# Kernel optimization log

Measured on AMD Instinct MI355X. Metric: run time of the kernel, lower is better.

The kernel has to match this reference:

```python
import jax, jax.numpy as jnp
import numpy as np

N_EMBD = 2048
QKV_EMBD = 2048
N_HEAD = 32
N_KV_HEAD = 8
HEAD_DIM = QKV_EMBD // N_HEAD  # 64
GROUPS = N_HEAD // N_KV_HEAD   # 4
ROPE_THETA = 10000.0
SCALE = float(np.sqrt(HEAD_DIM))


def setup_inputs() -> dict:
    key = jax.random.key(0)
    ks = jax.random.split(key, 12)
    B, S = 2, 2048
    inp = {
        "query": jax.random.normal(ks[0], (B, S, N_EMBD), jnp.float32),
        "key": jax.random.normal(ks[1], (B, S, N_EMBD), jnp.float32),
        "value": jax.random.normal(ks[2], (B, S, N_EMBD), jnp.float32),
        "mask": jnp.ones((B, S), dtype=bool),
        "Wq": jax.random.normal(ks[3], (QKV_EMBD, N_EMBD), jnp.float32) * 0.02,
        "bq": jnp.zeros((QKV_EMBD,), jnp.float32),
        "Wk": jax.random.normal(ks[4], (N_KV_HEAD * HEAD_DIM, N_EMBD), jnp.float32) * 0.02,
        "bk": jnp.zeros((N_KV_HEAD * HEAD_DIM,), jnp.float32),
        "Wv": jax.random.normal(ks[5], (N_KV_HEAD * HEAD_DIM, N_EMBD), jnp.float32) * 0.02,
        "bv": jnp.zeros((N_KV_HEAD * HEAD_DIM,), jnp.float32),
        "Wo": jax.random.normal(ks[6], (N_EMBD, QKV_EMBD), jnp.float32) * 0.02,
        "bo": jnp.zeros((N_EMBD,), jnp.float32),
    }
    return inp


def _rotate_half(x):
    d = x.shape[-1] // 2
    return jnp.concatenate([-x[..., d:], x[..., :d]], axis=-1)


def _rope_cos_sin(seq_len, dtype):
    # rope_factor == 1.0 -> no NTK adjustment; is_causal -> position_ids = arange
    inv_freq = 1.0 / (ROPE_THETA ** (jnp.arange(0, HEAD_DIM, 2, dtype=jnp.float32) / HEAD_DIM))
    pos = jnp.arange(seq_len, dtype=jnp.float32)
    freqs = jnp.einsum("i,j->ij", pos, inv_freq)           # [S, D/2]
    emb = jnp.concatenate([freqs, freqs], axis=-1)          # [S, D]
    return jnp.cos(emb).astype(dtype)[None, None], jnp.sin(emb).astype(dtype)[None, None]


def reference(query, key, value, mask, Wq, bq, Wk, bk, Wv, bv, Wo, bo):
    B, S, _ = query.shape
    Q = (query @ Wq.T + bq).reshape(B, S, N_HEAD, HEAD_DIM).transpose(0, 2, 1, 3)      # [B,H,S,D]
    K = (key @ Wk.T + bk).reshape(B, S, N_KV_HEAD, HEAD_DIM).transpose(0, 2, 1, 3)     # [B,KV,S,D]
    V = (value @ Wv.T + bv).reshape(B, S, N_KV_HEAD, HEAD_DIM).transpose(0, 2, 1, 3)

    cos, sin = _rope_cos_sin(S, Q.dtype)
    Q = Q * cos + _rotate_half(Q) * sin
    K = K * cos + _rotate_half(K) * sin

    # interleaved GQA repeat: each kv head serves GROUPS consecutive query heads
    K = jnp.repeat(K, GROUPS, axis=1)  # [B,H,S,D]
    V = jnp.repeat(V, GROUPS, axis=1)

    attn = jnp.einsum("bhqd,bhkd->bhqk", Q, K)              # [B,H,S,S]
    causal = jnp.tril(jnp.ones((S, S), dtype=bool))
    full_mask = mask[:, None, None, :] & causal[None, None]  # [B,1,S,S]
    attn = jnp.where(full_mask, attn, jnp.finfo(attn.dtype).min)
    attn_weights = jax.nn.softmax(attn / SCALE, axis=-1)     # dropout p=0 (eval)
    out = jnp.einsum("bhqk,bhkd->bhqd", attn_weights, V)
    out = out.transpose(0, 2, 1, 3).reshape(B, S, QKV_EMBD)
    return out @ Wo.T + bo
```

## Files before the change

### kernel.cpp

```cpp
#include <hip/hip_runtime.h>
#include <hip/hip_bf16.h>
#include <cmath>

#define NE   2048
#define NH   32
#define NKV  8
#define HD   64
#define SEQ  2048
#define NB   2

typedef __attribute__((ext_vector_type(4))) float f32x4;
typedef __attribute__((ext_vector_type(16))) float f32x16;
typedef __attribute__((ext_vector_type(8))) short bf16x8;
typedef __attribute__((ext_vector_type(4))) short bf16x4;

typedef const __attribute__((address_space(1))) void cgvoid;
typedef __attribute__((address_space(3))) void lvoid;

#define QSCALE 0.18033688011112042f

__device__ __forceinline__ short f2bf(float f) {
  union { float f; unsigned u; } v; v.f = f;
  unsigned r = v.u + 0x7fffu + ((v.u >> 16) & 1u);
  return (short)(r >> 16);
}

__device__ __forceinline__ unsigned cvt_pk_bf16(float a, float b) {
  unsigned r;
  asm("v_cvt_pk_bf16_f32 %0, %1, %2" : "=v"(r) : "v"(a), "v"(b));
  return r;
}

__global__ __launch_bounds__(256) void cvt_all(
    const float* __restrict__ s0, short* __restrict__ d0,
    const float* __restrict__ s1, short* __restrict__ d1,
    const float* __restrict__ s2, short* __restrict__ d2,
    const float* __restrict__ s3, short* __restrict__ d3,
    const float* __restrict__ s4, short* __restrict__ d4,
    const float* __restrict__ s5, short* __restrict__ d5,
    const float* __restrict__ s6, short* __restrict__ d6)
{
  int idx = blockIdx.x * 256 + threadIdx.x;
  const float* s; short* d; int rel;
  if      (idx < 1048576) { s = s0; d = d0; rel = idx; }
  else if (idx < 2097152) { s = s1; d = d1; rel = idx - 1048576; }
  else if (idx < 3145728) { s = s2; d = d2; rel = idx - 2097152; }
  else if (idx < 3670016) { s = s3; d = d3; rel = idx - 3145728; }
  else if (idx < 3801088) { s = s4; d = d4; rel = idx - 3670016; }
  else if (idx < 3932160) { s = s5; d = d5; rel = idx - 3801088; }
  else                    { s = s6; d = d6; rel = idx - 3932160; }
  size_t off = (size_t)rel * 8;
  f32x4 a = *(const f32x4*)(s + off);
  f32x4 b = *(const f32x4*)(s + off + 4);
  bf16x8 o;
  #pragma unroll
  for (int j = 0; j < 4; ++j) { o[j] = f2bf(a[j]); o[4 + j] = f2bf(b[j]); }
  *(bf16x8*)(d + off) = o;
}

template<int EPI>
__device__ __forceinline__ void gemm_body(
    short* As, short* Ws, int m0, int n0,
    const short* __restrict__ A, const short* __restrict__ W,
    const float* __restrict__ bias, void* __restrict__ Cout,
    int N, int K)
{
  const int t = threadIdx.x, lane = t & 63, w = t >> 6;
  const int lr = lane & 15, lg = lane >> 4;
  const int wm = (w >> 1) * 64, wn = (w & 1) * 64;

  f32x4 acc[4][4];
  #pragma unroll
  for (int i = 0; i < 4; ++i)
    #pragma unroll
    for (int j = 0; j < 4; ++j) acc[i][j] = (f32x4){0.f, 0.f, 0.f, 0.f};

  const int nt = K >> 6;

  #pragma unroll
  for (int it = 0; it < 4; ++it) {
    int e = it * 256 + t, r = e >> 3, c = e & 7;
    int cs = ((c ^ (r & 7)) << 3);
    __builtin_amdgcn_global_load_lds((cgvoid*)(A + (size_t)(m0 + r) * K + cs),
                                     (lvoid*)(As + e * 8), 16, 0, 0);
    __builtin_amdgcn_global_load_lds((cgvoid*)(W + (size_t)(n0 + r) * K + cs),
                                     (lvoid*)(Ws + e * 8), 16, 0, 0);
  }

  for (int ti = 0; ti < nt; ++ti) {
    const int cur = ti & 1;
    const short* Ab = As + cur * 8192;
    const short* Wb = Ws + cur * 8192;
    if (ti + 1 < nt) {
      const int k0 = (ti + 1) << 6;
      short* An = As + (cur ^ 1) * 8192;
      short* Wn = Ws + (cur ^ 1) * 8192;
      #pragma unroll
      for (int it = 0; it < 4; ++it) {
        int e = it * 256 + t, r = e >> 3, c = e & 7;
        int cs = ((c ^ (r & 7)) << 3);
        __builtin_amdgcn_global_load_lds((cgvoid*)(A + (size_t)(m0 + r) * K + k0 + cs),
                                         (lvoid*)(An + e * 8), 16, 0, 0);
        __builtin_amdgcn_global_load_lds((cgvoid*)(W + (size_t)(n0 + r) * K + k0 + cs),
                                         (lvoid*)(Wn + e * 8), 16, 0, 0);
      }
      asm volatile("s_waitcnt vmcnt(8)" ::: "memory");
    } else {
      asm volatile("s_waitcnt vmcnt(0)" ::: "memory");
    }
    __builtin_amdgcn_s_barrier();

    bf16x8 af[2][4], wf[2][4];
    #pragma unroll
    for (int ks = 0; ks < 2; ++ks)
      #pragma unroll
      for (int mf = 0; mf < 4; ++mf) {
        int row = wm + mf * 16 + lr;
        af[ks][mf] = *(const bf16x8*)(Ab + row * 64 + (((ks * 4 + lg) ^ (row & 7)) << 3));
      }
    #pragma unroll
    for (int ks = 0; ks < 2; ++ks)
      #pragma unroll
      for (int nf = 0; nf < 4; ++nf) {
        int row = wn + nf * 16 + lr;
        wf[ks][nf] = *(const bf16x8*)(Wb + row * 64 + (((ks * 4 + lg) ^ (row & 7)) << 3));
      }
    __builtin_amdgcn_s_setprio(1);
    #pragma unroll
    for (int ks = 0; ks < 2; ++ks)
      #pragma unroll
      for (int mf = 0; mf < 4; ++mf)
        #pragma unroll
        for (int nf = 0; nf < 4; ++nf)
          acc[mf][nf] = __builtin_amdgcn_mfma_f32_16x16x32_bf16(af[ks][mf], wf[ks][nf], acc[mf][nf], 0, 0, 0);
    __builtin_amdgcn_s_setprio(0);
    __builtin_amdgcn_s_barrier();
  }

  if (EPI == 0) {
    float* C = (float*)Cout;
    #pragma unroll
    for (int mf = 0; mf < 4; ++mf)
      #pragma unroll
      for (int nf = 0; nf < 4; ++nf)
        #pragma unroll
        for (int i = 0; i < 4; ++i) {
          int m = m0 + wm + mf * 16 + lg * 4 + i;
          int n = n0 + wn + nf * 16 + lr;
          C[(size_t)m * N + n] = acc[mf][nf][i] + bias[n];
        }
  } else if (EPI == 1) {
    short* C = (short*)Cout;
    #pragma unroll
    for (int mf = 0; mf < 4; ++mf)
      #pragma unroll
      for (int nf = 0; nf < 4; ++nf) {
        int n = n0 + wn + nf * 16 + lr;
        int kv = n >> 6, d = n & 63;
        int mb = m0 + wm + mf * 16 + lg * 4;
        int b = mb >> 11, s = mb & (SEQ - 1);
        bf16x4 pb;
        #pragma unroll
        for (int i = 0; i < 4; ++i) pb[i] = f2bf(acc[mf][nf][i] + bias[n]);
        *(bf16x4*)(C + (((size_t)b * NKV + kv) * HD + d) * SEQ + s) = pb;
      }
  } else {
    const int HN = (EPI == 2) ? NH : NKV;
    short* C = (short*)Cout;
    #pragma unroll
    for (int mf = 0; mf < 4; ++mf)
      #pragma unroll
      for (int nf2 = 0; nf2 < 2; ++nf2)
        #pragma unroll
        for (int i = 0; i < 4; ++i) {
          int m = m0 + wm + mf * 16 + lg * 4 + i;
          int b = m >> 11, s = m & (SEQ - 1);
          int n1 = n0 + wn + nf2 * 16 + lr;
          int n2 = n1 + 32;
          float v1 = acc[mf][nf2][i] + bias[n1];
          float v2 = acc[mf][nf2 + 2][i] + bias[n2];
          int d1 = n1 & 63;
          float inv = exp2f(-(float)d1 * (13.287712379549449f / 32.0f));
          float ang = (float)s * inv;
          float c, sn;
          __sincosf(ang, &sn, &c);
          float o1 = v1 * c - v2 * sn;
          float o2 = v2 * c + v1 * sn;
          if (EPI == 2) { o1 *= QSCALE; o2 *= QSCALE; }
          int h = n1 >> 6;
          size_t base = (((size_t)b * HN + h) * SEQ + s) * HD;
          C[base + d1]      = f2bf(o1);
          C[base + d1 + 32] = f2bf(o2);
        }
  }
}

template<int EPI>
__global__ __launch_bounds__(256) void gemm_bf16(
    const short* __restrict__ A, const short* __restrict__ W,
    const float* __restrict__ bias, void* __restrict__ Cout, int N, int K)
{
  __shared__ __align__(16) short As[2 * 128 * 64];
  __shared__ __align__(16) short Ws[2 * 128 * 64];
  gemm_body<EPI>(As, Ws, blockIdx.x * 128, blockIdx.y * 128, A, W, bias, Cout, N, K);
}

__global__ __launch_bounds__(256) void gemm_qkv(
    const short* __restrict__ qA, const short* __restrict__ Wq,
    const float* __restrict__ bq, short* __restrict__ Qout,
    const short* __restrict__ kA, const short* __restrict__ Wk,
    const float* __restrict__ bk, short* __restrict__ Kout,
    const short* __restrict__ vA, const short* __restrict__ Wv,
    const float* __restrict__ bv, short* __restrict__ Vout)
{
  __shared__ __align__(16) short As[2 * 128 * 64];
  __shared__ __align__(16) short Ws[2 * 128 * 64];
  int bid = blockIdx.x;
  if (bid < 512) {
    gemm_body<2>(As, Ws, (bid & 31) * 128, (bid >> 5) * 128, qA, Wq, bq, (void*)Qout, NE, NE);
  } else if (bid < 640) {
    int b2 = bid - 512;
    gemm_body<3>(As, Ws, (b2 & 31) * 128, (b2 >> 5) * 128, kA, Wk, bk, (void*)Kout, NKV * HD, NE);
  } else {
    int b2 = bid - 640;
    gemm_body<1>(As, Ws, (b2 & 31) * 128, (b2 >> 5) * 128, vA, Wv, bv, (void*)Vout, NKV * HD, NE);
  }
}

__global__ __launch_bounds__(256) void attn_kernel(
    const short* __restrict__ Q, const short* __restrict__ K,
    const short* __restrict__ Vt, short* __restrict__ O)
{
  __shared__ __align__(16) short Ks[2][64 * 64];
  __shared__ __align__(16) short Vs[2][64 * 64];

  const int t = threadIdx.x, lane = t & 63, w = t >> 6;
  const int l31 = lane & 31, hi = lane >> 5;
  const int by = blockIdx.y;
  const int b = by >> 3, kvh = by & 7;
  const int h = kvh * 4 + w;

  const short* Qh = Q + ((size_t)b * NH + h) * SEQ * HD;
  const short* Kh = K + ((size_t)b * NKV + kvh) * SEQ * HD;
  const short* Vh = Vt + ((size_t)b * NKV + kvh) * (size_t)HD * SEQ;

  #pragma unroll 1
  for (int pass = 0; pass < 2; ++pass) {
    const int qb32 = pass ? blockIdx.x : (63 - blockIdx.x);
    const int q0 = qb32 * 32;
    const int ntile = (qb32 >> 1) + 1;
    const int qpos = q0 + l31;

    bf16x8 qfr[4];
    #pragma unroll
    for (int dd = 0; dd < 4; ++dd)
      qfr[dd] = *(const bf16x8*)(Qh + (size_t)(q0 + l31) * HD + dd * 16 + hi * 8);

    f32x16 o[2];
    #pragma unroll
    for (int dh = 0; dh < 2; ++dh)
      #pragma unroll
      for (int r = 0; r < 16; ++r) o[dh][r] = 0.f;
    float lsum = 0.f;

    #pragma unroll
    for (int it = 0; it < 2; ++it) {
      int cid = it * 256 + t;
      int r = cid >> 3, c = cid & 7;
      int cs = ((c ^ (r & 7)) << 3);
      __builtin_amdgcn_global_load_lds((cgvoid*)(Kh + (size_t)r * HD + cs),
                                       (lvoid*)(Ks[0] + cid * 8), 16, 0, 0);
      __builtin_amdgcn_global_load_lds((cgvoid*)(Vh + (size_t)r * SEQ + cs),
                                       (lvoid*)(Vs[0] + cid * 8), 16, 0, 0);
    }
    __syncthreads();

    for (int ti = 0; ti < ntile; ++ti) {
      const int cur = ti & 1;
      if (ti + 1 < ntile) {
        const int kvn = (ti + 1) * 64;
        #pragma unroll
        for (int it = 0; it < 2; ++it) {
          int cid = it * 256 + t;
          int r = cid >> 3, c = cid & 7;
          int cs = ((c ^ (r & 7)) << 3);
          __builtin_amdgcn_global_load_lds((cgvoid*)(Kh + (size_t)(kvn + r) * HD + cs),
                                           (lvoid*)(Ks[cur ^ 1] + cid * 8), 16, 0, 0);
          __builtin_amdgcn_global_load_lds((cgvoid*)(Vh + (size_t)r * SEQ + kvn + cs),
                                           (lvoid*)(Vs[cur ^ 1] + cid * 8), 16, 0, 0);
        }
      }
      const int kv0 = ti * 64;
      const short* Kb = Ks[cur];
      const short* Vb = Vs[cur];

      f32x16 p[2];
      __builtin_amdgcn_s_setprio(1);
      #pragma unroll
      for (int f = 0; f < 2; ++f) {
        f32x16 z;
        #pragma unroll
        for (int r = 0; r < 16; ++r) z[r] = 0.f;
        #pragma unroll
        for (int dd = 0; dd < 4; ++dd) {
          int row = f * 32 + l31;
          bf16x8 ka = *(const bf16x8*)(Kb + row * 64 + (((2 * dd + hi) ^ (row & 7)) << 3));
          z = __builtin_amdgcn_mfma_f32_32x32x16_bf16(ka, qfr[dd], z, 0, 0, 0);
        }
        p[f] = z;
      }
      __builtin_amdgcn_s_setprio(0);

      if (ti == ntile - 1) {
        #pragma unroll
        for (int f = 0; f < 2; ++f)
          #pragma unroll
          for (int r = 0; r < 16; ++r) {
            int kpos = kv0 + f * 32 + (r & 3) + 8 * (r >> 2) + 4 * hi;
            if (kpos > qpos) p[f][r] = -INFINITY;
          }
      }

      unsigned pa[4][4];
      #pragma unroll
      for (int f = 0; f < 2; ++f) {
        float e[16];
        #pragma unroll
        for (int r = 0; r < 16; ++r) {
          e[r] = __builtin_amdgcn_exp2f(p[f][r]);
          lsum += e[r];
        }
        unsigned c[8];
        #pragma unroll
        for (int i = 0; i < 8; ++i) c[i] = cvt_pk_bf16(e[2 * i], e[2 * i + 1]);
        asm volatile("v_permlane32_swap_b32 %0, %1" : "+v"(c[0]), "+v"(c[2]));
        asm volatile("v_permlane32_swap_b32 %0, %1" : "+v"(c[1]), "+v"(c[3]));
        asm volatile("v_permlane32_swap_b32 %0, %1" : "+v"(c[4]), "+v"(c[6]));
        asm volatile("v_permlane32_swap_b32 %0, %1" : "+v"(c[5]), "+v"(c[7]));
        pa[2 * f][0] = c[0]; pa[2 * f][1] = c[1]; pa[2 * f][2] = c[2]; pa[2 * f][3] = c[3];
        pa[2 * f + 1][0] = c[4]; pa[2 * f + 1][1] = c[5];
        pa[2 * f + 1][2] = c[6]; pa[2 * f + 1][3] = c[7];
      }

      __builtin_amdgcn_s_setprio(1);
      #pragma unroll
      for (int ks = 0; ks < 4; ++ks) {
        bf16x8 paf = *(const bf16x8*)&pa[ks][0];
        #pragma unroll
        for (int dh = 0; dh < 2; ++dh) {
          int row = dh * 32 + l31;
          bf16x8 vb = *(const bf16x8*)(Vb + row * 64 + (((2 * ks + hi) ^ (row & 7)) << 3));
          o[dh] = __builtin_amdgcn_mfma_f32_32x32x16_bf16(paf, vb, o[dh], 0, 0, 0);
        }
      }
      __builtin_amdgcn_s_setprio(0);
      __syncthreads();
    }

    lsum += __shfl_xor(lsum, 32);
    #pragma unroll
    for (int r = 0; r < 16; ++r) {
      int crow = (r & 3) + 8 * (r >> 2) + 4 * hi;
      float li = __shfl(lsum, crow, 64);
      float invl = 1.0f / li;
      int s = q0 + crow;
      size_t base = (((size_t)b * SEQ + s) * NH + h) * HD;
      O[base + l31]      = f2bf(o[0][r] * invl);
      O[base + 32 + l31] = f2bf(o[1][r] * invl);
    }
  }
}

extern "C" void kernel_launch(void* const* d_in, const int* in_sizes, int n_in,
                              void* d_out, int out_size, void* d_ws, size_t ws_size,
                              hipStream_t stream) {
  (void)in_sizes; (void)n_in; (void)out_size; (void)ws_size;
  const float* q  = (const float*)d_in[0];
  const float* k  = (const float*)d_in[1];
  const float* v  = (const float*)d_in[2];
  const float* Wq = (const float*)d_in[4];
  const float* bq = (const float*)d_in[5];
  const float* Wk = (const float*)d_in[6];
  const float* bk = (const float*)d_in[7];
  const float* Wv = (const float*)d_in[8];
  const float* bv = (const float*)d_in[9];
  const float* Wo = (const float*)d_in[10];
  const float* bo = (const float*)d_in[11];

  const size_t SQ2 = (size_t)NB * SEQ * NE;
  const size_t W1  = (size_t)NE * NE;
  const size_t W2  = (size_t)(NKV * HD) * NE;
  const size_t KVN = (size_t)NB * NKV * SEQ * HD;

  short* ws = (short*)d_ws;
  short* qb  = ws;
  short* kb  = ws + SQ2;
  short* vb  = ws + 2 * SQ2;
  short* Wqb = ws + 3 * SQ2;
  short* Wkb = Wqb + W1;
  short* Wvb = Wkb + W2;
  short* Wob = Wvb + W2;
  short* Qr  = Wob + W1;
  short* Kr  = Qr + SQ2;
  short* Vr  = Kr + KVN;
  short* Ob  = qb;

  dim3 blk(256);

  cvt_all<<<17408, blk, 0, stream>>>(q, qb, k, kb, v, vb, Wq, Wqb, Wk, Wkb, Wv, Wvb, Wo, Wob);
  gemm_qkv<<<768, blk, 0, stream>>>(qb, Wqb, bq, Qr, kb, Wkb, bk, Kr, vb, Wvb, bv, Vr);
  attn_kernel<<<dim3(32, NB * NKV), blk, 0, stream>>>(Qr, Kr, Vr, Ob);
  gemm_bf16<0><<<dim3(32, 16), blk, 0, stream>>>(Ob, Wob, bo, d_out, NE, NE);
}
```

Measured before the change: 216.1 us.

## Use 256x256 tiles with 512-thread blocks for fused QKV projection GEMM

Replaces the 128x128-tile QKV GEMM (768 blocks of 256 threads) with a 256x256-tile version (192 blocks of 512 threads, 8 waves each computing 128x64). A lambda issues the double-buffered async global-to-LDS loads, and a partial vmcnt wait lets the next stage's loads stay in flight during compute. Block indices are remapped so neighbouring blocks are spread across the XCDs, and the RoPE frequency computation is hoisted out of the inner epilogue loop. Larger tiles raise arithmetic intensity and cut redundant operand loads, at the cost of fewer blocks, which can underfill the 256 CUs, plus more registers and LDS per block.

```diff
diff --git a/kernel.cpp b/kernel.cpp
--- a/kernel.cpp
+++ b/kernel.cpp
@@ -59,15 +59,162 @@
 }
 
 template<int EPI>
-__device__ __forceinline__ void gemm_body(
+__device__ __forceinline__ void gemm256_body(
     short* As, short* Ws, int m0, int n0,
     const short* __restrict__ A, const short* __restrict__ W,
-    const float* __restrict__ bias, void* __restrict__ Cout,
-    int N, int K)
+    const float* __restrict__ bias, void* __restrict__ Cout, int K)
 {
   const int t = threadIdx.x, lane = t & 63, w = t >> 6;
   const int lr = lane & 15, lg = lane >> 4;
+  const int wm = (w >> 2) * 128, wn = (w & 3) * 64;
+
+  f32x4 acc[8][4];
+  #pragma unroll
+  for (int i = 0; i < 8; ++i)
+    #pragma unroll
+    for (int j = 0; j < 4; ++j) acc[i][j] = (f32x4){0.f, 0.f, 0.f, 0.f};
+
+  auto STAGE = [&](int kt) {
+    const int k0 = kt << 6;
+    short* Ad = As + (kt & 1) * 16384;
+    short* Wd = Ws + (kt & 1) * 16384;
+    #pragma unroll
+    for (int it = 0; it < 4; ++it) {
+      int e = it * 512 + t, r = e >> 3, c = e & 7;
+      int cs = ((c ^ (r & 7)) << 3);
+      __builtin_amdgcn_global_load_lds((cgvoid*)(A + (size_t)(m0 + r) * K + k0 + cs),
+                                       (lvoid*)(Ad + e * 8), 16, 0, 0);
+      __builtin_amdgcn_global_load_lds((cgvoid*)(W + (size_t)(n0 + r) * K + k0 + cs),
+                                       (lvoid*)(Wd + e * 8), 16, 0, 0);
+    }
+  };
+
+  const int nt = K >> 6;
+  STAGE(0);
+
+  for (int ti = 0; ti < nt; ++ti) {
+    const short* Ab = As + (ti & 1) * 16384;
+    const short* Wb = Ws + (ti & 1) * 16384;
+    if (ti + 1 < nt) {
+      STAGE(ti + 1);
+      asm volatile("s_waitcnt vmcnt(8)" ::: "memory");
+    } else {
+      asm volatile("s_waitcnt vmcnt(0)" ::: "memory");
+    }
+    __builtin_amdgcn_s_barrier();
+
+    bf16x8 wf[2][4];
+    #pragma unroll
+    for (int ks = 0; ks < 2; ++ks)
+      #pragma unroll
+      for (int nf = 0; nf < 4; ++nf) {
+        int row = wn + nf * 16 + lr;
+        wf[ks][nf] = *(const bf16x8*)(Wb + row * 64 + (((ks * 4 + lg) ^ (row & 7)) << 3));
+      }
+    #pragma unroll
+    for (int mq = 0; mq < 4; ++mq) {
+      bf16x8 af[2][2];
+      #pragma unroll
+      for (int ks = 0; ks < 2; ++ks)
+        #pragma unroll
+        for (int mi = 0; mi < 2; ++mi) {
+          int row = wm + (mq * 2 + mi) * 16 + lr;
+          af[ks][mi] = *(const bf16x8*)(Ab + row * 64 + (((ks * 4 + lg) ^ (row & 7)) << 3));
+        }
+      __builtin_amdgcn_s_setprio(1);
+      #pragma unroll
+      for (int ks = 0; ks < 2; ++ks)
+        #pragma unroll
+        for (int mi = 0; mi < 2; ++mi)
+          #pragma unroll
+          for (int nf = 0; nf < 4; ++nf)
+            acc[mq * 2 + mi][nf] =
+                __builtin_amdgcn_mfma_f32_16x16x32_bf16(af[ks][mi], wf[ks][nf],
+                                                        acc[mq * 2 + mi][nf], 0, 0, 0);
+      __builtin_amdgcn_s_setprio(0);
+    }
+    __builtin_amdgcn_s_barrier();
+  }
+
+  if (EPI == 1) {
+    short* C = (short*)Cout;
+    #pragma unroll
+    for (int mf = 0; mf < 8; ++mf)
+      #pragma unroll
+      for (int nf = 0; nf < 4; ++nf) {
+        int n = n0 + wn + nf * 16 + lr;
+        int kv = n >> 6, d = n & 63;
+        int mb = m0 + wm + mf * 16 + lg * 4;
+        int b = mb >> 11, s = mb & (SEQ - 1);
+        bf16x4 pb;
+        #pragma unroll
+        for (int i = 0; i < 4; ++i) pb[i] = f2bf(acc[mf][nf][i] + bias[n]);
+        *(bf16x4*)(C + (((size_t)b * NKV + kv) * HD + d) * SEQ + s) = pb;
+      }
+  } else {
+    const int HN = (EPI == 2) ? NH : NKV;
+    short* C = (short*)Cout;
+    #pragma unroll
+    for (int mf = 0; mf < 8; ++mf)
+      #pragma unroll
+      for (int nf2 = 0; nf2 < 2; ++nf2) {
+        int n1 = n0 + wn + nf2 * 16 + lr;
+        int d1 = n1 & 63;
+        int h = n1 >> 6;
+        float inv = exp2f(-(float)d1 * (13.287712379549449f / 32.0f));
+        #pragma unroll
+        for (int i = 0; i < 4; ++i) {
+          int m = m0 + wm + mf * 16 + lg * 4 + i;
+          int b = m >> 11, s = m & (SEQ - 1);
+          float v1 = acc[mf][nf2][i] + bias[n1];
+          float v2 = acc[mf][nf2 + 2][i] + bias[n1 + 32];
+          float ang = (float)s * inv;
+          float c, sn;
+          __sincosf(ang, &sn, &c);
+          float o1 = v1 * c - v2 * sn;
+          float o2 = v2 * c + v1 * sn;
+          if (EPI == 2) { o1 *= QSCALE; o2 *= QSCALE; }
+          size_t base = (((size_t)b * HN + h) * SEQ + s) * HD;
+          C[base + d1]      = f2bf(o1);
+          C[base + d1 + 32] = f2bf(o2);
+        }
+      }
+  }
+}
+
+__global__ __launch_bounds__(512, 2) void gemm_qkv256(
+    const short* __restrict__ qA, const short* __restrict__ Wq,
+    const float* __restrict__ bq, short* __restrict__ Qout,
+    const short* __restrict__ kA, const short* __restrict__ Wk,
+    const float* __restrict__ bk, short* __restrict__ Kout,
+    const short* __restrict__ vA, const short* __restrict__ Wv,
+    const float* __restrict__ bv, short* __restrict__ Vout)
+{
+  __shared__ __align__(16) short As[2 * 256 * 64];
+  __shared__ __align__(16) short Ws[2 * 256 * 64];
+  int orig = blockIdx.x;
+  int bid = (orig & 7) * 24 + (orig >> 3);
+  if (bid < 128) {
+    gemm256_body<2>(As, Ws, (bid & 15) * 256, (bid >> 4) * 256, qA, Wq, bq, (void*)Qout, NE);
+  } else if (bid < 160) {
+    int b2 = bid - 128;
+    gemm256_body<3>(As, Ws, (b2 & 15) * 256, (b2 >> 4) * 256, kA, Wk, bk, (void*)Kout, NE);
+  } else {
+    int b2 = bid - 160;
+    gemm256_body<1>(As, Ws, (b2 & 15) * 256, (b2 >> 4) * 256, vA, Wv, bv, (void*)Vout, NE);
+  }
+}
+
+__global__ __launch_bounds__(256) void gemm_o(
+    const short* __restrict__ A, const short* __restrict__ W,
+    const float* __restrict__ bias, float* __restrict__ C, int N, int K)
+{
+  __shared__ __align__(16) short As[2 * 128 * 64];
+  __shared__ __align__(16) short Ws[2 * 128 * 64];
+  const int t = threadIdx.x, lane = t & 63, w = t >> 6;
+  const int lr = lane & 15, lg = lane >> 4;
   const int wm = (w >> 1) * 64, wn = (w & 1) * 64;
+  const int m0 = blockIdx.x * 128, n0 = blockIdx.y * 128;
 
   f32x4 acc[4][4];
   #pragma unroll
@@ -76,7 +223,6 @@
     for (int j = 0; j < 4; ++j) acc[i][j] = (f32x4){0.f, 0.f, 0.f, 0.f};
 
   const int nt = K >> 6;
-
   #pragma unroll
   for (int it = 0; it < 4; ++it) {
     int e = it * 256 + t, r = e >> 3, c = e & 7;
@@ -137,94 +283,16 @@
     __builtin_amdgcn_s_barrier();
   }
 
-  if (EPI == 0) {
-    float* C = (float*)Cout;
-    #pragma unroll
-    for (int mf = 0; mf < 4; ++mf)
-      #pragma unroll
-      for (int nf = 0; nf < 4; ++nf)
-        #pragma unroll
-        for (int i = 0; i < 4; ++i) {
-          int m = m0 + wm + mf * 16 + lg * 4 + i;
-          int n = n0 + wn + nf * 16 + lr;
-          C[(size_t)m * N + n] = acc[mf][nf][i] + bias[n];
-        }
-  } else if (EPI == 1) {
-    short* C = (short*)Cout;
-    #pragma unroll
-    for (int mf = 0; mf < 4; ++mf)
-      #pragma unroll
-      for (int nf = 0; nf < 4; ++nf) {
+  #pragma unroll
+  for (int mf = 0; mf < 4; ++mf)
+    #pragma unroll
+    for (int nf = 0; nf < 4; ++nf)
+      #pragma unroll
+      for (int i = 0; i < 4; ++i) {
+        int m = m0 + wm + mf * 16 + lg * 4 + i;
         int n = n0 + wn + nf * 16 + lr;
-        int kv = n >> 6, d = n & 63;
-        int mb = m0 + wm + mf * 16 + lg * 4;
-        int b = mb >> 11, s = mb & (SEQ - 1);
-        bf16x4 pb;
-        #pragma unroll
-        for (int i = 0; i < 4; ++i) pb[i] = f2bf(acc[mf][nf][i] + bias[n]);
-        *(bf16x4*)(C + (((size_t)b * NKV + kv) * HD + d) * SEQ + s) = pb;
-      }
-  } else {
-    const int HN = (EPI == 2) ? NH : NKV;
-    short* C = (short*)Cout;
-    #pragma unroll
-    for (int mf = 0; mf < 4; ++mf)
-      #pragma unroll
-      for (int nf2 = 0; nf2 < 2; ++nf2)
-        #pragma unroll
-        for (int i = 0; i < 4; ++i) {
-          int m = m0 + wm + mf * 16 + lg * 4 + i;
-          int b = m >> 11, s = m & (SEQ - 1);
-          int n1 = n0 + wn + nf2 * 16 + lr;
-          int n2 = n1 + 32;
-          float v1 = acc[mf][nf2][i] + bias[n1];
-          float v2 = acc[mf][nf2 + 2][i] + bias[n2];
-          int d1 = n1 & 63;
-          float inv = exp2f(-(float)d1 * (13.287712379549449f / 32.0f));
-          float ang = (float)s * inv;
-          float c, sn;
-          __sincosf(ang, &sn, &c);
-          float o1 = v1 * c - v2 * sn;
-          float o2 = v2 * c + v1 * sn;
-          if (EPI == 2) { o1 *= QSCALE; o2 *= QSCALE; }
-          int h = n1 >> 6;
-          size_t base = (((size_t)b * HN + h) * SEQ + s) * HD;
-          C[base + d1]      = f2bf(o1);
-          C[base + d1 + 32] = f2bf(o2);
-        }
-  }
-}
-
-template<int EPI>
-__global__ __launch_bounds__(256) void gemm_bf16(
-    const short* __restrict__ A, const short* __restrict__ W,
-    const float* __restrict__ bias, void* __restrict__ Cout, int N, int K)
-{
-  __shared__ __align__(16) short As[2 * 128 * 64];
-  __shared__ __align__(16) short Ws[2 * 128 * 64];
-  gemm_body<EPI>(As, Ws, blockIdx.x * 128, blockIdx.y * 128, A, W, bias, Cout, N, K);
-}
-
-__global__ __launch_bounds__(256) void gemm_qkv(
-    const short* __restrict__ qA, const short* __restrict__ Wq,
-    const float* __restrict__ bq, short* __restrict__ Qout,
-    const short* __restrict__ kA, const short* __restrict__ Wk,
-    const float* __restrict__ bk, short* __restrict__ Kout,
-    const short* __restrict__ vA, const short* __restrict__ Wv,
-    const float* __restrict__ bv, short* __restrict__ Vout)
-{
-  __shared__ __align__(16) short As[2 * 128 * 64];
-  __shared__ __align__(16) short Ws[2 * 128 * 64];
-  int bid = blockIdx.x;
-  if (bid < 512) {
-    gemm_body<2>(As, Ws, (bid & 31) * 128, (bid >> 5) * 128, qA, Wq, bq, (void*)Qout, NE, NE);
-  } else if (bid < 640) {
-    int b2 = bid - 512;
-    gemm_body<3>(As, Ws, (b2 & 31) * 128, (b2 >> 5) * 128, kA, Wk, bk, (void*)Kout, NKV * HD, NE);
-  } else {
-    int b2 = bid - 640;
-    gemm_body<1>(As, Ws, (b2 & 31) * 128, (b2 >> 5) * 128, vA, Wv, bv, (void*)Vout, NKV * HD, NE);
-  }
+        C[(size_t)m * N + n] = acc[mf][nf][i] + bias[n];
+      }
 }
 
 __global__ __launch_bounds__(256) void attn_kernel(
@@ -408,7 +476,7 @@
   dim3 blk(256);
 
   cvt_all<<<17408, blk, 0, stream>>>(q, qb, k, kb, v, vb, Wq, Wqb, Wk, Wkb, Wv, Wvb, Wo, Wob);
-  gemm_qkv<<<768, blk, 0, stream>>>(qb, Wqb, bq, Qr, kb, Wkb, bk, Kr, vb, Wvb, bv, Vr);
+  gemm_qkv256<<<192, dim3(512), 0, stream>>>(qb, Wqb, bq, Qr, kb, Wkb, bk, Kr, vb, Wvb, bv, Vr);
   attn_kernel<<<dim3(32, NB * NKV), blk, 0, stream>>>(Qr, Kr, Vr, Ob);
-  gemm_bf16<0><<<dim3(32, 16), blk, 0, stream>>>(Ob, Wob, bo, d_out, NE, NE);
-}
+  gemm_o<<<dim3(32, 16), blk, 0, stream>>>(Ob, Wob, bo, (float*)d_out, NE, NE);
+}
```

Result: faster. 206.9 us (-4.3%).
